# Kernel tuning notes

Hardware: AMD Instinct MI355X
Metric: run time of the kernel (lower is better)

The kernel has to match this reference:

```python
import jax, jax.numpy as jnp
import numpy as np
import math

N_NODES = 100000
N_EDGES = 1600000
IN_FEATS = 64
H_FEATS = 64
NUM_CLASSES = 2
LS_D = [2, 4, 6, 8]
LS_COEFF = [1.0, 1.0, 1.0, 1.0]
K = 4  # polynomial order per conv (len of each theta)


def _chi_theta(d, coeff):
    # Faithful port of calculate_theta_Chi for d > 0: fit chi-square-like
    # density on [0,2] with a degree-3 Chebyshev series, reverse coeffs.
    n = 2 * d
    m = 1.0 / (n / 2 + 1)  # i = n/2 - 1, m = 1/(i+2)
    def y(x):
        x = np.asarray(x, dtype=np.float64)
        return 1.0 / (2 ** (n / 2) * math.gamma(n / 2)) * (x / m) ** (n / 2 - 1) * np.exp(-(x / m) / 2)
    xs = np.linspace(0.0, 2.0, 20001)
    S = np.trapz(y(xs), xs)  # dense trapezoid ~ scipy.integrate.quad on [0,2]
    lambs = np.linspace(0.0, 2.0, 500)
    c = np.polynomial.chebyshev.chebfit(lambs, y(lambs) / S, 3)
    return (c[::-1] * coeff).astype(np.float32)

THETAS_NP = np.stack([_chi_theta(d, c) for d, c in zip(LS_D, LS_COEFF)])  # [4, K]


def setup_inputs() -> dict:
    key = jax.random.key(0)
    ks = jax.random.split(key, 8)
    sc = 0.05
    return {
        "x": jax.random.normal(ks[0], (N_NODES, IN_FEATS), dtype=jnp.float32),
        "src": jax.random.randint(ks[1], (N_EDGES,), 0, N_NODES, dtype=jnp.int32),
        "dst": jax.random.randint(ks[2], (N_EDGES,), 0, N_NODES, dtype=jnp.int32),
        "thetas": jnp.asarray(THETAS_NP),
        "W1": jax.random.normal(ks[3], (IN_FEATS, H_FEATS), dtype=jnp.float32) * sc,
        "b1": jnp.zeros((H_FEATS,), dtype=jnp.float32),
        "W2": jax.random.normal(ks[4], (H_FEATS, H_FEATS), dtype=jnp.float32) * sc,
        "b2": jnp.zeros((H_FEATS,), dtype=jnp.float32),
        "Wm1": jax.random.normal(ks[5], (H_FEATS * len(LS_D), H_FEATS), dtype=jnp.float32) * sc,
        "bm1": jnp.zeros((H_FEATS,), dtype=jnp.float32),
        "Wm2": jax.random.normal(ks[6], (H_FEATS, NUM_CLASSES), dtype=jnp.float32) * sc,
        "bm2": jnp.zeros((NUM_CLASSES,), dtype=jnp.float32),
    }


def reference(x, src, dst, thetas, W1, b1, W2, b2, Wm1, bm1, Wm2, bm2):
    n = x.shape[0]
    # input MLP stem
    h = jax.nn.relu(x @ W1 + b1)
    h = jax.nn.relu(h @ W2 + b2)
    # D^{-1/2} from in-degrees (clamped to >= 1), as in DGL in_degrees()
    deg = jax.ops.segment_sum(jnp.ones_like(dst, dtype=h.dtype), dst, num_segments=n)
    dinv = jnp.maximum(deg, 1.0) ** -0.5  # [N]
    dinv = dinv[:, None]  # [N, 1]
    # shared Laplacian power sequence: feats[k] = L^k h with L = I - D^-1/2 A D^-1/2
    feats = [h]
    f = h
    for _ in range(K - 1):
        t = f * dinv                                   # [N, H]
        agg = jax.ops.segment_sum(t[src], dst, num_segments=n)  # gather-scatter SpMM
        f = f - agg * dinv
        feats.append(f)
    F = jnp.stack(feats)  # [K, N, H]
    # per-conv polynomial combination, then concat along feature dim
    h_final = jnp.einsum('ck,knh->nch', thetas, F).reshape(n, -1)  # [N, C*H]
    # output MLP (2 layers)
    h_out = jax.nn.relu(h_final @ Wm1 + bm1)
    return h_out @ Wm2 + bm2
```

## Files before the change

### kernel.cpp

```cpp
#include <hip/hip_runtime.h>
#include <math.h>

#define FS3 192
#define TS  256
#define BCAP2 4608
#define CHUNK 4096
#define FTHREADS 768
#define FROWS 192

__device__ __forceinline__ void fma4(float4& a, float s, const float4& b) {
    a.x = fmaf(s, b.x, a.x);
    a.y = fmaf(s, b.y, a.y);
    a.z = fmaf(s, b.z, a.z);
    a.w = fmaf(s, b.w, a.w);
}

__device__ __forceinline__ unsigned short f2bf(float f) {
    unsigned int u = __builtin_bit_cast(unsigned int, f);
    u += 0x7fff + ((u >> 16) & 1);
    return (unsigned short)(u >> 16);
}
__device__ __forceinline__ float bf2f(unsigned short s) {
    return __builtin_bit_cast(float, ((unsigned int)s) << 16);
}
__device__ __forceinline__ float bflo(unsigned int u) {
    return __builtin_bit_cast(float, u << 16);
}
__device__ __forceinline__ float bfhi(unsigned int u) {
    return __builtin_bit_cast(float, u & 0xffff0000u);
}

__global__ void zero_k(int* __restrict__ p, int n) {
    int i = blockIdx.x * blockDim.x + threadIdx.x;
    int st = gridDim.x * blockDim.x;
    for (; i < n; i += st) p[i] = 0;
}

__global__ __launch_bounds__(256) void part1_k(const int* __restrict__ src,
        const int* __restrict__ dst, int* __restrict__ gcnt,
        unsigned int* __restrict__ pairs, int E, int NB) {
    __shared__ int lcnt[512];
    __shared__ int lbase[512];
    __shared__ int lpos[512];
    int tid = threadIdx.x;
    int base = blockIdx.x * CHUNK;
    int m = E - base; if (m > CHUNK) m = CHUNK;
    for (int b = tid; b < NB; b += 256) { lcnt[b] = 0; lpos[b] = 0; }
    __syncthreads();
    for (int i = tid; i < m; i += 256)
        atomicAdd(&lcnt[dst[base + i] >> 8], 1);
    __syncthreads();
    for (int b = tid; b < NB; b += 256)
        lbase[b] = (lcnt[b] > 0) ? atomicAdd(&gcnt[b], lcnt[b]) : 0;
    __syncthreads();
    for (int i = tid; i < m; i += 256) {
        int s = src[base + i], d = dst[base + i];
        int b = d >> 8;
        int p = atomicAdd(&lpos[b], 1);
        int idx = lbase[b] + p;
        if (idx < BCAP2)
            pairs[(size_t)b * BCAP2 + idx] = (unsigned int)s | ((unsigned int)(d & 255) << 17);
    }
}

__global__ __launch_bounds__(512) void bscan_k(const int* __restrict__ gcnt,
        int* __restrict__ bbase, int* __restrict__ rowp, int NB, int E, int n) {
    __shared__ int buf[512];
    int tid = threadIdx.x;
    int v = (tid < NB) ? (gcnt[tid] > BCAP2 ? BCAP2 : gcnt[tid]) : 0;
    buf[tid] = v;
    __syncthreads();
    int x = v;
    for (int off = 1; off < 512; off <<= 1) {
        int t = (tid >= off) ? buf[tid - off] : 0;
        __syncthreads();
        x += t;
        buf[tid] = x;
        __syncthreads();
    }
    if (tid < NB) bbase[tid] = x - v;
    if (tid == 0) rowp[n] = E;
}

__global__ __launch_bounds__(256) void csr2_k(const int* __restrict__ gcnt,
        const unsigned int* __restrict__ pairs, const int* __restrict__ bbase,
        int* __restrict__ rowp, int* __restrict__ colb, float* __restrict__ dinv, int n) {
    int b = blockIdx.x;
    int tid = threadIdx.x;
    int cntb = gcnt[b]; if (cntb > BCAP2) cntb = BCAP2;
    const unsigned int* pb = pairs + (size_t)b * BCAP2;
    __shared__ int c[256];
    __shared__ int sc[256];
    __shared__ int lpos[256];
    c[tid] = 0; lpos[tid] = 0;
    __syncthreads();
    for (int i = tid; i < cntb; i += 256)
        atomicAdd(&c[pb[i] >> 17], 1);
    __syncthreads();
    int v = c[tid];
    sc[tid] = v;
    __syncthreads();
    int x = v;
    for (int off = 1; off < 256; off <<= 1) {
        int t = (tid >= off) ? sc[tid - off] : 0;
        __syncthreads();
        x += t;
        sc[tid] = x;
        __syncthreads();
    }
    int ex = x - v;
    sc[tid] = ex;
    int node = b * 256 + tid;
    if (node < n) {
        rowp[node] = bbase[b] + ex;
        dinv[node] = 1.0f / sqrtf((float)(v > 1 ? v : 1));
    }
    __syncthreads();
    for (int i = tid; i < cntb; i += 256) {
        unsigned int pk = pb[i];
        int j = pk >> 17;
        int p = atomicAdd(&lpos[j], 1);
        colb[bbase[b] + sc[j] + p] = (int)(pk & 0x1FFFF);
    }
}

__global__ __launch_bounds__(256) void mlp_k(const float* __restrict__ x,
        const float* __restrict__ W1, const float* __restrict__ b1,
        const float* __restrict__ W2, const float* __restrict__ b2,
        const float* __restrict__ dinv,
        float* __restrict__ F, unsigned short* __restrict__ Tcat, int n, int ntiles) {
    __shared__ float Ws1[64 * 64];
    __shared__ float Ws2[64 * 64];
    __shared__ float xT[64 * 68];
    int tid = threadIdx.x;
    int ti = tid >> 4, tj = tid & 15;
    for (int idx = tid; idx < 4096; idx += 256) { Ws1[idx] = W1[idx]; Ws2[idx] = W2[idx]; }
    float4 b1v = *(const float4*)&b1[4 * tj];
    float4 b2v = *(const float4*)&b2[4 * tj];

    for (int g = blockIdx.x; g < ntiles; g += gridDim.x) {
        int base = g * 64;
        __syncthreads();
        for (int it = 0; it < 4; it++) {
            int node = ti + it * 16;
            int gn = base + node;
            float4 v = make_float4(0.f, 0.f, 0.f, 0.f);
            if (gn < n) v = *(const float4*)&x[(size_t)gn * 64 + 4 * tj];
            xT[(4 * tj + 0) * 68 + node] = v.x;
            xT[(4 * tj + 1) * 68 + node] = v.y;
            xT[(4 * tj + 2) * 68 + node] = v.z;
            xT[(4 * tj + 3) * 68 + node] = v.w;
        }
        __syncthreads();

        float4 a0 = b1v, a1 = b1v, a2 = b1v, a3 = b1v;
        #pragma unroll 8
        for (int k = 0; k < 64; k++) {
            float4 xv = *(const float4*)&xT[k * 68 + 4 * ti];
            float4 wv = *(const float4*)&Ws1[k * 64 + 4 * tj];
            fma4(a0, xv.x, wv); fma4(a1, xv.y, wv); fma4(a2, xv.z, wv); fma4(a3, xv.w, wv);
        }
        __syncthreads();
        {
            int hb = (4 * tj) * 68 + 4 * ti;
            xT[hb + 0 * 68 + 0] = fmaxf(a0.x, 0.f);
            xT[hb + 1 * 68 + 0] = fmaxf(a0.y, 0.f);
            xT[hb + 2 * 68 + 0] = fmaxf(a0.z, 0.f);
            xT[hb + 3 * 68 + 0] = fmaxf(a0.w, 0.f);
            xT[hb + 0 * 68 + 1] = fmaxf(a1.x, 0.f);
            xT[hb + 1 * 68 + 1] = fmaxf(a1.y, 0.f);
            xT[hb + 2 * 68 + 1] = fmaxf(a1.z, 0.f);
            xT[hb + 3 * 68 + 1] = fmaxf(a1.w, 0.f);
            xT[hb + 0 * 68 + 2] = fmaxf(a2.x, 0.f);
            xT[hb + 1 * 68 + 2] = fmaxf(a2.y, 0.f);
            xT[hb + 2 * 68 + 2] = fmaxf(a2.z, 0.f);
            xT[hb + 3 * 68 + 2] = fmaxf(a2.w, 0.f);
            xT[hb + 0 * 68 + 3] = fmaxf(a3.x, 0.f);
            xT[hb + 1 * 68 + 3] = fmaxf(a3.y, 0.f);
            xT[hb + 2 * 68 + 3] = fmaxf(a3.z, 0.f);
            xT[hb + 3 * 68 + 3] = fmaxf(a3.w, 0.f);
        }
        __syncthreads();

        a0 = b2v; a1 = b2v; a2 = b2v; a3 = b2v;
        #pragma unroll 8
        for (int k = 0; k < 64; k++) {
            float4 xv = *(const float4*)&xT[k * 68 + 4 * ti];
            float4 wv = *(const float4*)&Ws2[k * 64 + 4 * tj];
            fma4(a0, xv.x, wv); fma4(a1, xv.y, wv); fma4(a2, xv.z, wv); fma4(a3, xv.w, wv);
        }
        int gn0 = base + 4 * ti;
#define STORE_ROW(ai, ii)                                                                  \
        {                                                                                  \
            int gn = gn0 + (ii);                                                           \
            if (gn < n) {                                                                  \
                float r0 = fmaxf(ai.x, 0.f), r1 = fmaxf(ai.y, 0.f);                        \
                float r2 = fmaxf(ai.z, 0.f), r3 = fmaxf(ai.w, 0.f);                        \
                *(float4*)&F[(size_t)gn * FS3 + 4 * tj] = make_float4(r0, r1, r2, r3);     \
                float dg = dinv[gn];                                                       \
                ushort4 tv;                                                                \
                tv.x = f2bf(r0 * dg); tv.y = f2bf(r1 * dg);                                \
                tv.z = f2bf(r2 * dg); tv.w = f2bf(r3 * dg);                                \
                *(ushort4*)&Tcat[(size_t)gn * TS + 4 * tj] = tv;                           \
            }                                                                              \
        }
        STORE_ROW(a0, 0) STORE_ROW(a1, 1) STORE_ROW(a2, 2) STORE_ROW(a3, 3)
#undef STORE_ROW
    }
}

__global__ void wm1p_k(const float* __restrict__ thetas, const float* __restrict__ Wm1,
                       float* __restrict__ Wm1p) {
    int idx = blockIdx.x * blockDim.x + threadIdx.x;
    if (idx >= 16384) return;
    int j = idx & 63;
    int q = idx >> 6;
    int k = q >> 6;
    int hh = q & 63;
    float a = 0.f;
    for (int c = 0; c < 4; c++) a += thetas[c * 4 + k] * Wm1[(c * 64 + hh) * 64 + j];
    Wm1p[idx] = a;
}

__global__ __launch_bounds__(256) void prop_k(const float* __restrict__ Fin,
        float* __restrict__ Fout,
        const unsigned short* __restrict__ Tin, unsigned short* __restrict__ Tout,
        const int* __restrict__ rowp, const int* __restrict__ colb,
        const float* __restrict__ dinv, int n, int writeF) {
    int w = (blockIdx.x * blockDim.x + threadIdx.x) >> 6;
    int lane = threadIdx.x & 63;
    int nA = 2 * w, nB = 2 * w + 1;
    if (nA >= n) return;
    bool hasB = (nB < n);
    int eA = rowp[nA], endA = rowp[nA + 1];
    int eB = 0, endB = 0;
    if (hasB) { eB = rowp[nB]; endB = rowp[nB + 1]; }
    float a0 = 0.f, a1 = 0.f, b0 = 0.f, b1 = 0.f;
    while (eA + 3 < endA && eB + 3 < endB) {
        int sA0 = colb[eA], sA1 = colb[eA + 1], sA2 = colb[eA + 2], sA3 = colb[eA + 3];
        int sB0 = colb[eB], sB1 = colb[eB + 1], sB2 = colb[eB + 2], sB3 = colb[eB + 3];
        float fA0 = bf2f(Tin[(size_t)sA0 * TS + lane]);
        float fA1 = bf2f(Tin[(size_t)sA1 * TS + lane]);
        float fA2 = bf2f(Tin[(size_t)sA2 * TS + lane]);
        float fA3 = bf2f(Tin[(size_t)sA3 * TS + lane]);
        float fB0 = bf2f(Tin[(size_t)sB0 * TS + lane]);
        float fB1 = bf2f(Tin[(size_t)sB1 * TS + lane]);
        float fB2 = bf2f(Tin[(size_t)sB2 * TS + lane]);
        float fB3 = bf2f(Tin[(size_t)sB3 * TS + lane]);
        a0 += fA0 + fA2; a1 += fA1 + fA3;
        b0 += fB0 + fB2; b1 += fB1 + fB3;
        eA += 4; eB += 4;
    }
    while (eA + 3 < endA) {
        int s0 = colb[eA], s1 = colb[eA + 1], s2 = colb[eA + 2], s3 = colb[eA + 3];
        float f0 = bf2f(Tin[(size_t)s0 * TS + lane]);
        float f1 = bf2f(Tin[(size_t)s1 * TS + lane]);
        float f2 = bf2f(Tin[(size_t)s2 * TS + lane]);
        float f3 = bf2f(Tin[(size_t)s3 * TS + lane]);
        a0 += f0 + f2; a1 += f1 + f3;
        eA += 4;
    }
    while (eB + 3 < endB) {
        int s0 = colb[eB], s1 = colb[eB + 1], s2 = colb[eB + 2], s3 = colb[eB + 3];
        float f0 = bf2f(Tin[(size_t)s0 * TS + lane]);
        float f1 = bf2f(Tin[(size_t)s1 * TS + lane]);
        float f2 = bf2f(Tin[(size_t)s2 * TS + lane]);
        float f3 = bf2f(Tin[(size_t)s3 * TS + lane]);
        b0 += f0 + f2; b1 += f1 + f3;
        eB += 4;
    }
    for (; eA < endA; ++eA) a0 += bf2f(Tin[(size_t)colb[eA] * TS + lane]);
    for (; eB < endB; ++eB) b0 += bf2f(Tin[(size_t)colb[eB] * TS + lane]);

    {
        float acc = a0 + a1;
        float dg = dinv[nA];
        float fo = Fin[(size_t)nA * FS3 + lane] - acc * dg;
        if (writeF) Fout[(size_t)nA * FS3 + lane] = fo;
        Tout[(size_t)nA * TS + lane] = f2bf(fo * dg);
    }
    if (hasB) {
        float acc = b0 + b1;
        float dg = dinv[nB];
        float fo = Fin[(size_t)nB * FS3 + lane] - acc * dg;
        if (writeF) Fout[(size_t)nB * FS3 + lane] = fo;
        Tout[(size_t)nB * TS + lane] = f2bf(fo * dg);
    }
}

__global__ __launch_bounds__(FTHREADS, 6) void final_k(const unsigned short* __restrict__ Tcat,
        const float* __restrict__ dinv,
        const float* __restrict__ Wm1p, const float* __restrict__ bm1,
        const float* __restrict__ Wm2, const float* __restrict__ bm2,
        float* __restrict__ out, int n, int ntiles) {
    __shared__ float Ws[256 * 64];
    int tid = threadIdx.x;
    int ti = tid >> 4, tj = tid & 15;
    for (int idx = tid; idx < 16384; idx += FTHREADS) Ws[idx] = Wm1p[idx];
    float4 bv = *(const float4*)&bm1[4 * tj];
    float2 w2a = ((const float2*)Wm2)[4 * tj + 0];
    float2 w2b = ((const float2*)Wm2)[4 * tj + 1];
    float2 w2c = ((const float2*)Wm2)[4 * tj + 2];
    float2 w2d = ((const float2*)Wm2)[4 * tj + 3];
    float bo0 = bm2[0], bo1 = bm2[1];
    __syncthreads();

    for (int g = blockIdx.x; g < ntiles; g += gridDim.x) {
        int base = g * FROWS;
        const unsigned short* tr = &Tcat[(size_t)(base + 4 * ti) * TS];
        float4 a0 = make_float4(0.f, 0.f, 0.f, 0.f);
        float4 a1 = a0, a2 = a0, a3 = a0;
        #pragma unroll 4
        for (int k = 0; k < 256; k += 8) {
            float4 w0 = *(const float4*)&Ws[(k + 0) * 64 + 4 * tj];
            float4 w1 = *(const float4*)&Ws[(k + 1) * 64 + 4 * tj];
            float4 w2 = *(const float4*)&Ws[(k + 2) * 64 + 4 * tj];
            float4 w3 = *(const float4*)&Ws[(k + 3) * 64 + 4 * tj];
            float4 w4 = *(const float4*)&Ws[(k + 4) * 64 + 4 * tj];
            float4 w5 = *(const float4*)&Ws[(k + 5) * 64 + 4 * tj];
            float4 w6 = *(const float4*)&Ws[(k + 6) * 64 + 4 * tj];
            float4 w7 = *(const float4*)&Ws[(k + 7) * 64 + 4 * tj];
#define ROW(ai, ii)                                                              \
            {                                                                    \
                uint4 u = *(const uint4*)&tr[(size_t)(ii) * TS + k];             \
                fma4(ai, bflo(u.x), w0); fma4(ai, bfhi(u.x), w1);                \
                fma4(ai, bflo(u.y), w2); fma4(ai, bfhi(u.y), w3);                \
                fma4(ai, bflo(u.z), w4); fma4(ai, bfhi(u.z), w5);                \
                fma4(ai, bflo(u.w), w6); fma4(ai, bfhi(u.w), w7);                \
            }
            ROW(a0, 0) ROW(a1, 1) ROW(a2, 2) ROW(a3, 3)
#undef ROW
        }
#define EMIT(ai, ii)                                                             \
        {                                                                        \
            int node = base + 4 * ti + (ii);                                     \
            float s = (node < n) ? (1.0f / dinv[node]) : 0.f;                    \
            float h0 = fmaxf(fmaf(ai.x, s, bv.x), 0.f);                          \
            float h1 = fmaxf(fmaf(ai.y, s, bv.y), 0.f);                          \
            float h2 = fmaxf(fmaf(ai.z, s, bv.z), 0.f);                          \
            float h3 = fmaxf(fmaf(ai.w, s, bv.w), 0.f);                          \
            float o0 = h0 * w2a.x + h1 * w2b.x + h2 * w2c.x + h3 * w2d.x;        \
            float o1 = h0 * w2a.y + h1 * w2b.y + h2 * w2c.y + h3 * w2d.y;        \
            o0 += __shfl_xor(o0, 1); o1 += __shfl_xor(o1, 1);                    \
            o0 += __shfl_xor(o0, 2); o1 += __shfl_xor(o1, 2);                    \
            o0 += __shfl_xor(o0, 4); o1 += __shfl_xor(o1, 4);                    \
            o0 += __shfl_xor(o0, 8); o1 += __shfl_xor(o1, 8);                    \
            if (tj == 0 && node < n) { out[node * 2] = o0 + bo0;                 \
                                       out[node * 2 + 1] = o1 + bo1; }           \
        }
        EMIT(a0, 0) EMIT(a1, 1) EMIT(a2, 2) EMIT(a3, 3)
#undef EMIT
    }
}

extern "C" void kernel_launch(void* const* d_in, const int* in_sizes, int n_in,
                              void* d_out, int out_size, void* d_ws, size_t ws_size,
                              hipStream_t stream) {
    const float* x      = (const float*)d_in[0];
    const int*   src    = (const int*)d_in[1];
    const int*   dst    = (const int*)d_in[2];
    const float* thetas = (const float*)d_in[3];
    const float* W1     = (const float*)d_in[4];
    const float* b1     = (const float*)d_in[5];
    const float* W2     = (const float*)d_in[6];
    const float* b2     = (const float*)d_in[7];
    const float* Wm1    = (const float*)d_in[8];
    const float* bm1    = (const float*)d_in[9];
    const float* Wm2    = (const float*)d_in[10];
    const float* bm2    = (const float*)d_in[11];
    float* out = (float*)d_out;

    int n = in_sizes[0] / 64;
    int E = in_sizes[1];
    int ntiles  = (n + 63) / 64;
    int ntiles2 = (n + FROWS - 1) / FROWS;
    int NB = (n + 255) / 256;

    float* Fbuf  = (float*)d_ws;
    float* dinv  = Fbuf + (size_t)n * FS3;
    int*   rowp  = (int*)(dinv + n);
    int*   colb  = rowp + (n + 1);
    float* Wm1p  = (float*)(colb + E);
    int*   gcnt  = (int*)(Wm1p + 16384);
    int*   bbase = gcnt + NB;
    size_t uoff = (((size_t)(bbase + NB) - (size_t)d_ws) + 255) & ~(size_t)255;
    unsigned int*   pairs = (unsigned int*)((char*)d_ws + uoff);
    unsigned short* Tcat  = (unsigned short*)pairs;

    int nchunksP = (E + CHUNK - 1) / CHUNK;

    zero_k<<<4, 256, 0, stream>>>(gcnt, NB);
    part1_k<<<nchunksP, 256, 0, stream>>>(src, dst, gcnt, pairs, E, NB);
    bscan_k<<<1, 512, 0, stream>>>(gcnt, bbase, rowp, NB, E, n);
    csr2_k<<<NB, 256, 0, stream>>>(gcnt, pairs, bbase, rowp, colb, dinv, n);

    mlp_k<<<768, 256, 0, stream>>>(x, W1, b1, W2, b2, dinv, Fbuf, Tcat, n, ntiles);
    wm1p_k<<<64, 256, 0, stream>>>(thetas, Wm1, Wm1p);

    int nwaves = (n + 1) / 2;
    int pblocks = ((size_t)nwaves * 64 + 255) / 256;
    prop_k<<<pblocks, 256, 0, stream>>>(
        Fbuf + 0 * 64, Fbuf + 1 * 64, Tcat + 0 * 64, Tcat + 1 * 64, rowp, colb, dinv, n, 1);
    prop_k<<<pblocks, 256, 0, stream>>>(
        Fbuf + 1 * 64, Fbuf + 2 * 64, Tcat + 1 * 64, Tcat + 2 * 64, rowp, colb, dinv, n, 1);
    prop_k<<<pblocks, 256, 0, stream>>>(
        Fbuf + 2 * 64, Fbuf + 2 * 64, Tcat + 2 * 64, Tcat + 3 * 64, rowp, colb, dinv, n, 0);

    final_k<<<ntiles2, FTHREADS, 0, stream>>>(Tcat, dinv, Wm1p, bm1, Wm2, bm2, out, n, ntiles2);
}
```

Before: 308.5 us.

## Use bf16 MFMA with hi/lo split weights in final output MLP kernel

The final projection (256-wide bf16 Tcat times combined Wm1) now runs on the matrix cores via 16x16x32 bf16 MFMA instead of scalar FMAs against an LDS-resident fp32 weight tile. To keep precision, the fused weights are split into bf16 high and low parts and two MFMAs accumulate per k-step. Weights are held in registers, and per-column-group partial outputs are reduced through a small shared array. This removes the 64KB LDS weight staging and the FMA-bound inner loop, at the cost of twice the MFMA work and a different tiling with one 128-row tile per block.

```diff
diff --git a/kernel.cpp b/kernel.cpp
--- a/kernel.cpp
+++ b/kernel.cpp
@@ -5,29 +5,23 @@
 #define TS  256
 #define BCAP2 4608
 #define CHUNK 4096
-#define FTHREADS 768
-#define FROWS 192
-
+
+typedef __attribute__((ext_vector_type(8))) short short8v;
+typedef __attribute__((ext_vector_type(4))) float f32x4;
+
+__device__ __forceinline__ unsigned short f2bf(float f) {
+    unsigned int u = __builtin_bit_cast(unsigned int, f);
+    u += 0x7fff + ((u >> 16) & 1);
+    return (unsigned short)(u >> 16);
+}
+__device__ __forceinline__ float bf2f(unsigned short s) {
+    return __builtin_bit_cast(float, ((unsigned int)s) << 16);
+}
 __device__ __forceinline__ void fma4(float4& a, float s, const float4& b) {
     a.x = fmaf(s, b.x, a.x);
     a.y = fmaf(s, b.y, a.y);
     a.z = fmaf(s, b.z, a.z);
     a.w = fmaf(s, b.w, a.w);
-}
-
-__device__ __forceinline__ unsigned short f2bf(float f) {
-    unsigned int u = __builtin_bit_cast(unsigned int, f);
-    u += 0x7fff + ((u >> 16) & 1);
-    return (unsigned short)(u >> 16);
-}
-__device__ __forceinline__ float bf2f(unsigned short s) {
-    return __builtin_bit_cast(float, ((unsigned int)s) << 16);
-}
-__device__ __forceinline__ float bflo(unsigned int u) {
-    return __builtin_bit_cast(float, u << 16);
-}
-__device__ __forceinline__ float bfhi(unsigned int u) {
-    return __builtin_bit_cast(float, u & 0xffff0000u);
 }
 
 __global__ void zero_k(int* __restrict__ p, int n) {
@@ -210,7 +204,7 @@
 }
 
 __global__ void wm1p_k(const float* __restrict__ thetas, const float* __restrict__ Wm1,
-                       float* __restrict__ Wm1p) {
+                       unsigned short* __restrict__ Wth, unsigned short* __restrict__ Wtl) {
     int idx = blockIdx.x * blockDim.x + threadIdx.x;
     if (idx >= 16384) return;
     int j = idx & 63;
@@ -219,7 +213,10 @@
     int hh = q & 63;
     float a = 0.f;
     for (int c = 0; c < 4; c++) a += thetas[c * 4 + k] * Wm1[(c * 64 + hh) * 64 + j];
-    Wm1p[idx] = a;
+    unsigned short hi = f2bf(a);
+    float r = a - bf2f(hi);
+    Wth[j * 256 + q] = hi;
+    Wtl[j * 256 + q] = f2bf(r);
 }
 
 __global__ __launch_bounds__(256) void prop_k(const float* __restrict__ Fin,
@@ -288,68 +285,64 @@
     }
 }
 
-__global__ __launch_bounds__(FTHREADS, 6) void final_k(const unsigned short* __restrict__ Tcat,
+__global__ __launch_bounds__(512, 4) void final_k(const unsigned short* __restrict__ Tcat,
         const float* __restrict__ dinv,
-        const float* __restrict__ Wm1p, const float* __restrict__ bm1,
-        const float* __restrict__ Wm2, const float* __restrict__ bm2,
-        float* __restrict__ out, int n, int ntiles) {
-    __shared__ float Ws[256 * 64];
+        const unsigned short* __restrict__ Wth, const unsigned short* __restrict__ Wtl,
+        const float* __restrict__ bm1, const float* __restrict__ Wm2,
+        const float* __restrict__ bm2, float* __restrict__ out, int n) {
+    __shared__ float Lp[4][128][2];
     int tid = threadIdx.x;
-    int ti = tid >> 4, tj = tid & 15;
-    for (int idx = tid; idx < 16384; idx += FTHREADS) Ws[idx] = Wm1p[idx];
-    float4 bv = *(const float4*)&bm1[4 * tj];
-    float2 w2a = ((const float2*)Wm2)[4 * tj + 0];
-    float2 w2b = ((const float2*)Wm2)[4 * tj + 1];
-    float2 w2c = ((const float2*)Wm2)[4 * tj + 2];
-    float2 w2d = ((const float2*)Wm2)[4 * tj + 3];
-    float bo0 = bm2[0], bo1 = bm2[1];
-    __syncthreads();
-
-    for (int g = blockIdx.x; g < ntiles; g += gridDim.x) {
-        int base = g * FROWS;
-        const unsigned short* tr = &Tcat[(size_t)(base + 4 * ti) * TS];
-        float4 a0 = make_float4(0.f, 0.f, 0.f, 0.f);
-        float4 a1 = a0, a2 = a0, a3 = a0;
-        #pragma unroll 4
-        for (int k = 0; k < 256; k += 8) {
-            float4 w0 = *(const float4*)&Ws[(k + 0) * 64 + 4 * tj];
-            float4 w1 = *(const float4*)&Ws[(k + 1) * 64 + 4 * tj];
-            float4 w2 = *(const float4*)&Ws[(k + 2) * 64 + 4 * tj];
-            float4 w3 = *(const float4*)&Ws[(k + 3) * 64 + 4 * tj];
-            float4 w4 = *(const float4*)&Ws[(k + 4) * 64 + 4 * tj];
-            float4 w5 = *(const float4*)&Ws[(k + 5) * 64 + 4 * tj];
-            float4 w6 = *(const float4*)&Ws[(k + 6) * 64 + 4 * tj];
-            float4 w7 = *(const float4*)&Ws[(k + 7) * 64 + 4 * tj];
-#define ROW(ai, ii)                                                              \
-            {                                                                    \
-                uint4 u = *(const uint4*)&tr[(size_t)(ii) * TS + k];             \
-                fma4(ai, bflo(u.x), w0); fma4(ai, bfhi(u.x), w1);                \
-                fma4(ai, bflo(u.y), w2); fma4(ai, bfhi(u.y), w3);                \
-                fma4(ai, bflo(u.z), w4); fma4(ai, bfhi(u.z), w5);                \
-                fma4(ai, bflo(u.w), w6); fma4(ai, bfhi(u.w), w7);                \
+    int w = tid >> 6, l = tid & 63;
+    int cw = w & 3, half = w >> 2;
+    int colg = 16 * cw + (l & 15);
+    int krow = (l >> 4) * 8;
+
+    short8v bhi[8], blo[8];
+    #pragma unroll
+    for (int ks = 0; ks < 8; ks++) {
+        bhi[ks] = *(const short8v*)&Wth[colg * 256 + ks * 32 + krow];
+        blo[ks] = *(const short8v*)&Wtl[colg * 256 + ks * 32 + krow];
+    }
+    float bm1c = bm1[colg];
+    float w2x = Wm2[colg * 2 + 0], w2y = Wm2[colg * 2 + 1];
+
+    int gbase = blockIdx.x * 128 + half * 64;
+    const unsigned short* abase = &Tcat[(size_t)(gbase + (l & 15)) * TS + krow];
+
+    for (int rt = 0; rt < 4; rt++) {
+        f32x4 acc = {0.f, 0.f, 0.f, 0.f};
+        const unsigned short* ap = abase + (size_t)rt * 16 * TS;
+        #pragma unroll
+        for (int ks = 0; ks < 8; ks++) {
+            short8v a = *(const short8v*)(ap + ks * 32);
+            acc = __builtin_amdgcn_mfma_f32_16x16x32_bf16(a, bhi[ks], acc, 0, 0, 0);
+            acc = __builtin_amdgcn_mfma_f32_16x16x32_bf16(a, blo[ks], acc, 0, 0, 0);
+        }
+        #pragma unroll
+        for (int i = 0; i < 4; i++) {
+            int rl = half * 64 + rt * 16 + (l >> 4) * 4 + i;
+            int grow = blockIdx.x * 128 + rl;
+            float s = (grow < n) ? (1.0f / dinv[grow]) : 0.f;
+            float h = fmaxf(fmaf(acc[i], s, bm1c), 0.f);
+            float q0 = h * w2x, q1 = h * w2y;
+            q0 += __shfl_xor(q0, 1); q1 += __shfl_xor(q1, 1);
+            q0 += __shfl_xor(q0, 2); q1 += __shfl_xor(q1, 2);
+            q0 += __shfl_xor(q0, 4); q1 += __shfl_xor(q1, 4);
+            q0 += __shfl_xor(q0, 8); q1 += __shfl_xor(q1, 8);
+            if ((l & 15) == 0) {
+                Lp[cw][rl][0] = q0;
+                Lp[cw][rl][1] = q1;
             }
-            ROW(a0, 0) ROW(a1, 1) ROW(a2, 2) ROW(a3, 3)
-#undef ROW
-        }
-#define EMIT(ai, ii)                                                             \
-        {                                                                        \
-            int node = base + 4 * ti + (ii);                                     \
-            float s = (node < n) ? (1.0f / dinv[node]) : 0.f;                    \
-            float h0 = fmaxf(fmaf(ai.x, s, bv.x), 0.f);                          \
-            float h1 = fmaxf(fmaf(ai.y, s, bv.y), 0.f);                          \
-            float h2 = fmaxf(fmaf(ai.z, s, bv.z), 0.f);                          \
-            float h3 = fmaxf(fmaf(ai.w, s, bv.w), 0.f);                          \
-            float o0 = h0 * w2a.x + h1 * w2b.x + h2 * w2c.x + h3 * w2d.x;        \
-            float o1 = h0 * w2a.y + h1 * w2b.y + h2 * w2c.y + h3 * w2d.y;        \
-            o0 += __shfl_xor(o0, 1); o1 += __shfl_xor(o1, 1);                    \
-            o0 += __shfl_xor(o0, 2); o1 += __shfl_xor(o1, 2);                    \
-            o0 += __shfl_xor(o0, 4); o1 += __shfl_xor(o1, 4);                    \
-            o0 += __shfl_xor(o0, 8); o1 += __shfl_xor(o1, 8);                    \
-            if (tj == 0 && node < n) { out[node * 2] = o0 + bo0;                 \
-                                       out[node * 2 + 1] = o1 + bo1; }           \
-        }
-        EMIT(a0, 0) EMIT(a1, 1) EMIT(a2, 2) EMIT(a3, 3)
-#undef EMIT
+        }
+    }
+    __syncthreads();
+    if (tid < 256) {
+        int r = tid >> 1, ch = tid & 1;
+        int grow = blockIdx.x * 128 + r;
+        if (grow < n) {
+            float v = Lp[0][r][ch] + Lp[1][r][ch] + Lp[2][r][ch] + Lp[3][r][ch] + bm2[ch];
+            out[grow * 2 + ch] = v;
+        }
     }
 }
 
@@ -373,15 +366,17 @@
     int n = in_sizes[0] / 64;
     int E = in_sizes[1];
     int ntiles  = (n + 63) / 64;
-    int ntiles2 = (n + FROWS - 1) / FROWS;
+    int ntiles2 = (n + 127) / 128;
     int NB = (n + 255) / 256;
 
     float* Fbuf  = (float*)d_ws;
     float* dinv  = Fbuf + (size_t)n * FS3;
     int*   rowp  = (int*)(dinv + n);
     int*   colb  = rowp + (n + 1);
-    float* Wm1p  = (float*)(colb + E);
-    int*   gcnt  = (int*)(Wm1p + 16384);
+    size_t woff = (((size_t)(colb + E) - (size_t)d_ws) + 15) & ~(size_t)15;
+    unsigned short* Wth = (unsigned short*)((char*)d_ws + woff);
+    unsigned short* Wtl = Wth + 16384;
+    int*   gcnt  = (int*)(Wtl + 16384);
     int*   bbase = gcnt + NB;
     size_t uoff = (((size_t)(bbase + NB) - (size_t)d_ws) + 255) & ~(size_t)255;
     unsigned int*   pairs = (unsigned int*)((char*)d_ws + uoff);
@@ -395,7 +390,7 @@
     csr2_k<<<NB, 256, 0, stream>>>(gcnt, pairs, bbase, rowp, colb, dinv, n);
 
     mlp_k<<<768, 256, 0, stream>>>(x, W1, b1, W2, b2, dinv, Fbuf, Tcat, n, ntiles);
-    wm1p_k<<<64, 256, 0, stream>>>(thetas, Wm1, Wm1p);
+    wm1p_k<<<64, 256, 0, stream>>>(thetas, Wm1, Wth, Wtl);
 
     int nwaves = (n + 1) / 2;
     int pblocks = ((size_t)nwaves * 64 + 255) / 256;
@@ -406,5 +401,5 @@
     prop_k<<<pblocks, 256, 0, stream>>>(
         Fbuf + 2 * 64, Fbuf + 2 * 64, Tcat + 2 * 64, Tcat + 3 * 64, rowp, colb, dinv, n, 0);
 
-    final_k<<<ntiles2, FTHREADS, 0, stream>>>(Tcat, dinv, Wm1p, bm1, Wm2, bm2, out, n, ntiles2);
-}
+    final_k<<<ntiles2, 512, 0, stream>>>(Tcat, dinv, Wth, Wtl, bm1, Wm2, bm2, out, n);
+}
```

Measured after the change: 295.2 us. -4.3%, faster.
